# Kernel optimization log

Measured on AMD Instinct MI355X. Metric: run time of the kernel, lower is better.

The kernel has to match this reference:

```python
import jax, jax.numpy as jnp
import numpy as np

B, T, F_IN = 64, 512, 264        # batch, time, total features
NONLSTM = 8                      # trailing non-LSTM feature channels
F_LSTM = F_IN - NONLSTM          # 256 features fed to the LSTM stack
HIDDEN = [512, 512]              # stacked OptimizedLSTMCell dims
DENSE = [512, 256]
PRED, FPP = 16, 4                # predictions, features_per_prediction


def _glorot(key, shape):
    fan_in, fan_out = shape[0], shape[1]
    lim = jnp.sqrt(6.0 / (fan_in + fan_out))
    return jax.random.uniform(key, shape, jnp.float32, -lim, lim)


def setup_inputs() -> dict:
    key = jax.random.key(0)
    ks = jax.random.split(key, 16)
    inp = {"x": jax.random.normal(ks[0], (B, T, F_IN), jnp.float32)}
    # LSTM layer params: Wi [in,4H] (no bias on input proj), Wh [H,4H], b [4H]
    in_dim = F_LSTM
    for j, h in enumerate(HIDDEN):
        inp[f"Wi{j}"] = _glorot(ks[1 + 3 * j], (in_dim, 4 * h))
        inp[f"Wh{j}"] = _glorot(ks[2 + 3 * j], (h, 4 * h))
        inp[f"b{j}"] = jnp.zeros((4 * h,), jnp.float32)
        in_dim = h
    # Dense head
    d_in = HIDDEN[-1] + NONLSTM
    for i, d in enumerate(DENSE):
        inp[f"Wd{i}"] = _glorot(ks[8 + 2 * i], (d_in, d))
        inp[f"bd{i}"] = jnp.zeros((d,), jnp.float32)
        d_in = d
    inp["Wf"] = _glorot(ks[14], (d_in, PRED * FPP))
    inp["bf"] = jnp.zeros((PRED * FPP,), jnp.float32)
    return inp


def lstm_layer(x, Wi, Wh, b):
    """flax OptimizedLSTMCell scanned over time. x: [B, T, F] -> [B, T, H]."""
    Bq = x.shape[0]
    H = Wh.shape[0]
    xw = jnp.einsum('btf,fg->btg', x, Wi)  # precompute input projections

    def step(carry, z_in):
        c, h = carry
        z = z_in + h @ Wh + b
        i, f, g, o = jnp.split(z, 4, axis=-1)
        c = jax.nn.sigmoid(f) * c + jax.nn.sigmoid(i) * jnp.tanh(g)
        h = jax.nn.sigmoid(o) * jnp.tanh(c)
        return (c, h), h

    c0 = jnp.zeros((Bq, H), x.dtype)
    h0 = jnp.zeros((Bq, H), x.dtype)
    _, hs = jax.lax.scan(step, (c0, h0), jnp.swapaxes(xw, 0, 1))
    return jnp.swapaxes(hs, 0, 1)


def reference(x, Wi0, Wh0, b0, Wi1, Wh1, b1, Wd0, bd0, Wd1, bd1, Wf, bf):
    last_features = x[:, -1, -NONLSTM:]          # [B, 8]
    h = x[:, :, :-NONLSTM]                       # [B, T, 256]
    # single LSTM branch: history == T, downsample == 1
    h = lstm_layer(h, Wi0, Wh0, b0)
    h = lstm_layer(h, Wi1, Wh1, b1)
    out = h[:, -1, :]                            # [B, H]
    out = jnp.concatenate([out, last_features], axis=1)
    out = jax.nn.relu(out @ Wd0 + bd0)
    out = jax.nn.relu(out @ Wd1 + bd1)
    out = out @ Wf + bf
    out = out.reshape((-1, PRED, FPP))
    return jax.nn.sigmoid(out)
```

## Files before the change

### kernel.cpp

```cpp
#include <hip/hip_runtime.h>
#include <hip/hip_bf16.h>

typedef __hip_bfloat16 bf16;
typedef short bf16x8 __attribute__((ext_vector_type(8)));
typedef float f32x4 __attribute__((ext_vector_type(4)));
typedef unsigned long long u64;
typedef unsigned int u32;

#define MFMA16(A, B, C) __builtin_amdgcn_mfma_f32_16x16x32_bf16(A, B, C, 0, 0, 0)

__device__ __forceinline__ float sigf(float x) { return 1.f / (1.f + __expf(-x)); }
__device__ __forceinline__ float tanh_fast(float x) { return 2.f / (1.f + __expf(-2.f * x)) - 1.f; }

__device__ __forceinline__ bf16x8 ld16(const u64* p) {
  u64 lo = __hip_atomic_load(p, __ATOMIC_RELAXED, __HIP_MEMORY_SCOPE_SYSTEM);
  u64 hi = __hip_atomic_load(p + 1, __ATOMIC_RELAXED, __HIP_MEMORY_SCOPE_SYSTEM);
  union { u64 q[2]; bf16x8 v; } u;
  u.q[0] = lo; u.q[1] = hi;
  return u.v;
}

__global__ __launch_bounds__(256) void transpose_k(const float* __restrict__ W,
                                                   bf16* __restrict__ WT,
                                                   int K, int N) {
  __shared__ bf16 tile[32][33];
  const int n0 = blockIdx.x * 32, k0 = blockIdx.y * 32;
  const int c = threadIdx.x & 31, r0 = threadIdx.x >> 5;
  for (int i = 0; i < 4; ++i) {
    int r = r0 + 8 * i;
    tile[r][c] = __float2bfloat16(W[(long)(k0 + r) * N + (n0 + c)]);
  }
  __syncthreads();
  for (int i = 0; i < 4; ++i) {
    int r = r0 + 8 * i;
    WT[(long)(n0 + r) * K + (k0 + c)] = tile[c][r];
  }
}

__device__ __forceinline__ void gather16(const u64* __restrict__ mat, int m, int q,
                                         bf16x8* out) {
#pragma unroll
  for (int i = 0; i < 16; ++i) {
    const int s = i * 4 + q;
    out[i] = ld16(mat + ((long)(s << 6) + m) * 2);
  }
}

__global__ __launch_bounds__(256, 1) void lstm2_fused_k(
    const float* __restrict__ x,
    const bf16* __restrict__ WiT0, const bf16* __restrict__ WhT0,
    const float* __restrict__ bias0,
    const bf16* __restrict__ WiT1, const bf16* __restrict__ WhT1,
    const float* __restrict__ bias1,
    u64* __restrict__ h1D, u64* __restrict__ h2D,
    u32* __restrict__ sent)
{
  __shared__ short Wis[32 * 520];
  __shared__ short Whs[32 * 520];
  __shared__ float zs[32 * 66];
  __shared__ __align__(16) bf16 hstage[64 * 8];

  const int layer = blockIdx.x >> 6;
  const int w = blockIdx.x & 63;
  const int tid = threadIdx.x;
  const int lane = tid & 63;
  const int wv = tid >> 6;
  const int q = lane >> 4;
  const int r = lane & 15;

  const int K_in = layer ? 512 : 256;
  const bf16* WiT = layer ? WiT1 : WiT0;
  const bf16* WhT = layer ? WhT1 : WhT0;
  const float* bias = layer ? bias1 : bias0;
  u32* s0 = sent;
  u32* s1 = sent + 512 * 64;
  u64* hprevD = layer ? h2D : h1D;
  u64* houtD = layer ? h2D : h1D;
  u32* smy = (layer ? s1 : s0);

  for (int idx = tid; idx < 32 * 64; idx += 256) {
    const int j = idx >> 6, kc = idx & 63;
    const int zc = (j >> 3) * 512 + w * 8 + (j & 7);
    *(bf16x8*)(Whs + j * 520 + kc * 8) = *(const bf16x8*)(WhT + (long)zc * 512 + kc * 8);
  }
  const int csh = layer ? 6 : 5;
  const int cmask = (1 << csh) - 1;
  for (int idx = tid; idx < (32 << csh); idx += 256) {
    const int j = idx >> csh, kc = idx & cmask;
    const int zc = (j >> 3) * 512 + w * 8 + (j & 7);
    *(bf16x8*)(Wis + j * 520 + kc * 8) = *(const bf16x8*)(WiT + (long)zc * K_in + kc * 8);
  }

  const int m = wv * 16 + r;
  const short* wi0p = Wis + r * 520;
  const short* wi1p = Wis + (16 + r) * 520;
  const short* wh0p = Whs + r * 520;
  const short* wh1p = Whs + (16 + r) * 520;

  const int gb = tid & 63;
  const int gc0 = tid >> 6;
  float bias_r[2][4];
  for (int s = 0; s < 2; ++s)
    for (int g = 0; g < 4; ++g)
      bias_r[s][g] = bias[g * 512 + w * 8 + gc0 + 4 * s];
  float creg[2] = {0.f, 0.f};

  __syncthreads();

  for (int t = 0; t < 512; ++t) {
    f32x4 acc0 = {0.f, 0.f, 0.f, 0.f};
    f32x4 acc1 = {0.f, 0.f, 0.f, 0.f};

    if (layer == 0) {
      bf16x8 ax[8];
      const float* row = x + ((long)m * 512 + t) * 264;
#pragma unroll
      for (int i = 0; i < 8; ++i) {
        const float4 f0 = *(const float4*)(row + i * 32 + q * 8);
        const float4 f1 = *(const float4*)(row + i * 32 + q * 8 + 4);
        union { short s[8]; bf16x8 v8; } o;
        o.s[0] = __builtin_bit_cast(short, __float2bfloat16(f0.x));
        o.s[1] = __builtin_bit_cast(short, __float2bfloat16(f0.y));
        o.s[2] = __builtin_bit_cast(short, __float2bfloat16(f0.z));
        o.s[3] = __builtin_bit_cast(short, __float2bfloat16(f0.w));
        o.s[4] = __builtin_bit_cast(short, __float2bfloat16(f1.x));
        o.s[5] = __builtin_bit_cast(short, __float2bfloat16(f1.y));
        o.s[6] = __builtin_bit_cast(short, __float2bfloat16(f1.z));
        o.s[7] = __builtin_bit_cast(short, __float2bfloat16(f1.w));
        ax[i] = o.v8;
      }
#pragma unroll
      for (int i = 0; i < 8; ++i) {
        const int kk = i * 32;
        acc0 = MFMA16(ax[i], *(const bf16x8*)(wi0p + kk + q * 8), acc0);
        acc1 = MFMA16(ax[i], *(const bf16x8*)(wi1p + kk + q * 8), acc1);
      }
      if (t > 0) {
        if (tid < 64) {
          const u32* sp = s0 + (t - 1) * 64 + tid;
          while (__ballot(__hip_atomic_load(sp, __ATOMIC_RELAXED,
                                            __HIP_MEMORY_SCOPE_SYSTEM) != 0) != ~0ull)
            __builtin_amdgcn_s_sleep(2);
        }
        __syncthreads();
        bf16x8 ah[16];
        gather16(h1D + (long)(t - 1) * 8192, m, q, ah);
#pragma unroll
        for (int i = 0; i < 16; ++i) {
          const int kk = i * 32;
          acc0 = MFMA16(ah[i], *(const bf16x8*)(wh0p + kk + q * 8), acc0);
          acc1 = MFMA16(ah[i], *(const bf16x8*)(wh1p + kk + q * 8), acc1);
        }
      }
    } else {
      if (tid < 64) {
        const u32* sp = s0 + t * 64 + tid;
        while (__ballot(__hip_atomic_load(sp, __ATOMIC_RELAXED,
                                          __HIP_MEMORY_SCOPE_SYSTEM) != 0) != ~0ull)
          __builtin_amdgcn_s_sleep(2);
      }
      __syncthreads();
      bf16x8 ax[16];
      gather16(h1D + (long)t * 8192, m, q, ax);
#pragma unroll
      for (int i = 0; i < 16; ++i) {
        const int kk = i * 32;
        acc0 = MFMA16(ax[i], *(const bf16x8*)(wi0p + kk + q * 8), acc0);
        acc1 = MFMA16(ax[i], *(const bf16x8*)(wi1p + kk + q * 8), acc1);
      }
      if (t > 0) {
        if (tid < 64) {
          const u32* sp = s1 + (t - 1) * 64 + tid;
          while (__ballot(__hip_atomic_load(sp, __ATOMIC_RELAXED,
                                            __HIP_MEMORY_SCOPE_SYSTEM) != 0) != ~0ull)
            __builtin_amdgcn_s_sleep(2);
        }
        __syncthreads();
        bf16x8 ah[16];
        gather16(h2D + (long)(t - 1) * 8192, m, q, ah);
#pragma unroll
        for (int i = 0; i < 16; ++i) {
          const int kk = i * 32;
          acc0 = MFMA16(ah[i], *(const bf16x8*)(wh0p + kk + q * 8), acc0);
          acc1 = MFMA16(ah[i], *(const bf16x8*)(wh1p + kk + q * 8), acc1);
        }
      }
    }

    {
      const int brow = wv * 16 + q * 4;
      for (int i = 0; i < 4; ++i) zs[r * 66 + brow + i] = acc0[i];
      for (int i = 0; i < 4; ++i) zs[(16 + r) * 66 + brow + i] = acc1[i];
    }
    __syncthreads();

    for (int s = 0; s < 2; ++s) {
      const int c = gc0 + 4 * s;
      const float zi = zs[(c)*66 + gb] + bias_r[s][0];
      const float zf = zs[(8 + c) * 66 + gb] + bias_r[s][1];
      const float zg = zs[(16 + c) * 66 + gb] + bias_r[s][2];
      const float zo = zs[(24 + c) * 66 + gb] + bias_r[s][3];
      const float cnew = sigf(zf) * creg[s] + sigf(zi) * tanh_fast(zg);
      const float hnew = sigf(zo) * tanh_fast(cnew);
      creg[s] = cnew;
      hstage[gb * 8 + c] = __float2bfloat16(hnew);
    }
    __syncthreads();

    if (tid < 64) {
      const u64* src = (const u64*)(hstage + tid * 8);
      u64* dst = houtD + (((long)t * 64 + w) * 64 + tid) * 2;
      __hip_atomic_store(dst, src[0], __ATOMIC_RELAXED, __HIP_MEMORY_SCOPE_SYSTEM);
      __hip_atomic_store(dst + 1, src[1], __ATOMIC_RELAXED, __HIP_MEMORY_SCOPE_SYSTEM);
    }
    if (tid == 0)
      __hip_atomic_store(smy + t * 64 + w, 1u, __ATOMIC_RELEASE, __HIP_MEMORY_SCOPE_AGENT);
  }
}

__global__ __launch_bounds__(256) void head_k(
    const u64* __restrict__ h2D,
    const float* __restrict__ x,
    const float* __restrict__ Wd0, const float* __restrict__ bd0,
    const float* __restrict__ Wd1, const float* __restrict__ bd1,
    const float* __restrict__ Wf, const float* __restrict__ bfv,
    float* __restrict__ out) {
  const int b = blockIdx.x, tid = threadIdx.x;
  __shared__ float in0[520];
  __shared__ float d0s[512];
  __shared__ float d1s[256];
  if (tid < 64) {
    const int s = tid;
    bf16x8 v = ld16(h2D + (((long)511 * 64 + s) * 64 + b) * 2);
    union { bf16x8 v8; short sh[8]; } u;
    u.v8 = v;
    for (int j = 0; j < 8; ++j)
      in0[s * 8 + j] = __bfloat162float(__builtin_bit_cast(bf16, u.sh[j]));
  }
  if (tid < 8) in0[512 + tid] = x[((long)(b * 512 + 511)) * 264 + 256 + tid];
  __syncthreads();
  for (int j = tid; j < 512; j += 256) {
    float a = bd0[j];
    for (int k = 0; k < 520; ++k) a += in0[k] * Wd0[(long)k * 512 + j];
    d0s[j] = fmaxf(a, 0.f);
  }
  __syncthreads();
  if (tid < 256) {
    const int j = tid;
    float a = bd1[j];
    for (int k = 0; k < 512; ++k) a += d0s[k] * Wd1[(long)k * 256 + j];
    d1s[j] = fmaxf(a, 0.f);
  }
  __syncthreads();
  if (tid < 64) {
    const int j = tid;
    float a = bfv[j];
    for (int k = 0; k < 256; ++k) a += d1s[k] * Wf[(long)k * 64 + j];
    out[b * 64 + j] = sigf(a);
  }
}

extern "C" void kernel_launch(void* const* d_in, const int* in_sizes, int n_in,
                              void* d_out, int out_size, void* d_ws, size_t ws_size,
                              hipStream_t stream) {
  const float* x   = (const float*)d_in[0];
  const float* Wi0 = (const float*)d_in[1];
  const float* Wh0 = (const float*)d_in[2];
  const float* b0  = (const float*)d_in[3];
  const float* Wi1 = (const float*)d_in[4];
  const float* Wh1 = (const float*)d_in[5];
  const float* b1  = (const float*)d_in[6];
  const float* Wd0 = (const float*)d_in[7];
  const float* bd0 = (const float*)d_in[8];
  const float* Wd1 = (const float*)d_in[9];
  const float* bd1 = (const float*)d_in[10];
  const float* Wf  = (const float*)d_in[11];
  const float* bf_ = (const float*)d_in[12];
  float* out = (float*)d_out;

  char* ws = (char*)d_ws;
  size_t off = 0;
  auto carve = [&](size_t bytes) {
    void* p = ws + off;
    off += (bytes + 255) & ~(size_t)255;
    return p;
  };
  u32* sent = (u32*)carve((size_t)2 * 512 * 64 * 4);
  const size_t zero_bytes = off;
  bf16* WiT0 = (bf16*)carve((size_t)2048 * 256 * 2);
  bf16* WhT0 = (bf16*)carve((size_t)2048 * 512 * 2);
  bf16* WiT1 = (bf16*)carve((size_t)2048 * 512 * 2);
  bf16* WhT1 = (bf16*)carve((size_t)2048 * 512 * 2);
  u64*  h1D  = (u64*)carve((size_t)512 * 64 * 64 * 16);
  u64*  h2D  = (u64*)carve((size_t)512 * 64 * 64 * 16);

  hipMemsetAsync(sent, 0, zero_bytes, stream);

  transpose_k<<<dim3(2048 / 32, 256 / 32), 256, 0, stream>>>(Wi0, WiT0, 256, 2048);
  transpose_k<<<dim3(2048 / 32, 512 / 32), 256, 0, stream>>>(Wh0, WhT0, 512, 2048);
  transpose_k<<<dim3(2048 / 32, 512 / 32), 256, 0, stream>>>(Wi1, WiT1, 512, 2048);
  transpose_k<<<dim3(2048 / 32, 512 / 32), 256, 0, stream>>>(Wh1, WhT1, 512, 2048);

  lstm2_fused_k<<<128, 256, 0, stream>>>(x, WiT0, WhT0, b0, WiT1, WhT1, b1,
                                         h1D, h2D, sent);

  head_k<<<64, 256, 0, stream>>>(h2D, x, Wd0, bd0, Wd1, bd1, Wf, bf_, out);
}
```

Before: 2.954 ms.

## Split LSTM persistent kernel across batch groups with register-resident weights and split-K

The persistent two-layer LSTM kernel now runs 256 blocks instead of 128, partitioning work by layer, batch group (4 groups of 16) and 16-column gate slice. Each block syncs only on the 32 producer blocks of its own batch group rather than all 64. Recurrent weights, plus layer-0 input weights, are held in registers. The four waves split K and reduce partial sums through shared memory, and layer-1 input weights sit in XOR-swizzled LDS. The aim is to shorten the per-timestep critical path and cut the data gathered per step, at the cost of higher register pressure, more sentinels and a cross-wave reduction.

```diff
diff --git a/kernel.cpp b/kernel.cpp
--- a/kernel.cpp
+++ b/kernel.cpp
@@ -18,6 +18,19 @@
   union { u64 q[2]; bf16x8 v; } u;
   u.q[0] = lo; u.q[1] = hi;
   return u.v;
+}
+
+__device__ __forceinline__ bf16x8 pack8(float4 f0, float4 f1) {
+  union { short s[8]; bf16x8 v8; } o;
+  o.s[0] = __builtin_bit_cast(short, __float2bfloat16(f0.x));
+  o.s[1] = __builtin_bit_cast(short, __float2bfloat16(f0.y));
+  o.s[2] = __builtin_bit_cast(short, __float2bfloat16(f0.z));
+  o.s[3] = __builtin_bit_cast(short, __float2bfloat16(f0.w));
+  o.s[4] = __builtin_bit_cast(short, __float2bfloat16(f1.x));
+  o.s[5] = __builtin_bit_cast(short, __float2bfloat16(f1.y));
+  o.s[6] = __builtin_bit_cast(short, __float2bfloat16(f1.z));
+  o.s[7] = __builtin_bit_cast(short, __float2bfloat16(f1.w));
+  return o.v8;
 }
 
 __global__ __launch_bounds__(256) void transpose_k(const float* __restrict__ W,
@@ -37,15 +50,6 @@
   }
 }
 
-__device__ __forceinline__ void gather16(const u64* __restrict__ mat, int m, int q,
-                                         bf16x8* out) {
-#pragma unroll
-  for (int i = 0; i < 16; ++i) {
-    const int s = i * 4 + q;
-    out[i] = ld16(mat + ((long)(s << 6) + m) * 2);
-  }
-}
-
 __global__ __launch_bounds__(256, 1) void lstm2_fused_k(
     const float* __restrict__ x,
     const bf16* __restrict__ WiT0, const bf16* __restrict__ WhT0,
@@ -55,166 +59,174 @@
     u64* __restrict__ h1D, u64* __restrict__ h2D,
     u32* __restrict__ sent)
 {
-  __shared__ short Wis[32 * 520];
-  __shared__ short Whs[32 * 520];
-  __shared__ float zs[32 * 66];
-  __shared__ __align__(16) bf16 hstage[64 * 8];
-
-  const int layer = blockIdx.x >> 6;
-  const int w = blockIdx.x & 63;
+  __shared__ __align__(16) short Wi1s[64 * 512];
+  __shared__ float zs[4 * 64 * 20];
+  __shared__ __align__(16) bf16 hstage[256];
+
+  const int layer = blockIdx.x >> 7;
+  const int bg = (blockIdx.x >> 5) & 3;
+  const int cg = blockIdx.x & 31;
   const int tid = threadIdx.x;
   const int lane = tid & 63;
-  const int wv = tid >> 6;
+  const int kh = tid >> 6;
   const int q = lane >> 4;
   const int r = lane & 15;
 
-  const int K_in = layer ? 512 : 256;
-  const bf16* WiT = layer ? WiT1 : WiT0;
   const bf16* WhT = layer ? WhT1 : WhT0;
   const float* bias = layer ? bias1 : bias0;
   u32* s0 = sent;
-  u32* s1 = sent + 512 * 64;
-  u64* hprevD = layer ? h2D : h1D;
-  u64* houtD = layer ? h2D : h1D;
-  u32* smy = (layer ? s1 : s0);
-
-  for (int idx = tid; idx < 32 * 64; idx += 256) {
-    const int j = idx >> 6, kc = idx & 63;
-    const int zc = (j >> 3) * 512 + w * 8 + (j & 7);
-    *(bf16x8*)(Whs + j * 520 + kc * 8) = *(const bf16x8*)(WhT + (long)zc * 512 + kc * 8);
-  }
-  const int csh = layer ? 6 : 5;
-  const int cmask = (1 << csh) - 1;
-  for (int idx = tid; idx < (32 << csh); idx += 256) {
-    const int j = idx >> csh, kc = idx & cmask;
-    const int zc = (j >> 3) * 512 + w * 8 + (j & 7);
-    *(bf16x8*)(Wis + j * 520 + kc * 8) = *(const bf16x8*)(WiT + (long)zc * K_in + kc * 8);
-  }
-
-  const int m = wv * 16 + r;
-  const short* wi0p = Wis + r * 520;
-  const short* wi1p = Wis + (16 + r) * 520;
-  const short* wh0p = Whs + r * 520;
-  const short* wh1p = Whs + (16 + r) * 520;
-
-  const int gb = tid & 63;
-  const int gc0 = tid >> 6;
-  float bias_r[2][4];
-  for (int s = 0; s < 2; ++s)
-    for (int g = 0; g < 4; ++g)
-      bias_r[s][g] = bias[g * 512 + w * 8 + gc0 + 4 * s];
-  float creg[2] = {0.f, 0.f};
-
-  __syncthreads();
-
+  u32* s1 = sent + 512 * 128;
+  u32* smy = layer ? s1 : s0;
+  u64* hown = layer ? h2D : h1D;
+
+  bf16x8 wh[4][4];
+#pragma unroll
+  for (int nt = 0; nt < 4; ++nt)
+#pragma unroll
+    for (int kt = 0; kt < 4; ++kt)
+      wh[nt][kt] = *(const bf16x8*)(WhT + (long)(nt * 512 + cg * 16 + r) * 512 +
+                                    (kh * 4 + kt) * 32 + q * 8);
+
+  bf16x8 wi0r[4][2];
+  if (layer == 0) {
+#pragma unroll
+    for (int nt = 0; nt < 4; ++nt)
+#pragma unroll
+      for (int kt = 0; kt < 2; ++kt)
+        wi0r[nt][kt] = *(const bf16x8*)(WiT0 + (long)(nt * 512 + cg * 16 + r) * 256 +
+                                        (kh * 2 + kt) * 32 + q * 8);
+  } else {
+    char* wb = (char*)Wi1s;
+    for (int idx = tid; idx < 64 * 64; idx += 256) {
+      const int j = idx >> 6, kc = idx & 63;
+      const int col = (j >> 4) * 512 + cg * 16 + (j & 15);
+      *(bf16x8*)(wb + j * 1024 + ((kc ^ (j & 7)) * 16)) =
+          *(const bf16x8*)(WiT1 + (long)col * 512 + kc * 8);
+    }
+  }
+
+  const int erow = tid & 15, ec = tid >> 4;
+  float br[4];
+#pragma unroll
+  for (int g = 0; g < 4; ++g) br[g] = bias[g * 512 + cg * 16 + ec];
+  float creg = 0.f;
+
+  __syncthreads();
+
+#pragma unroll 1
   for (int t = 0; t < 512; ++t) {
-    f32x4 acc0 = {0.f, 0.f, 0.f, 0.f};
-    f32x4 acc1 = {0.f, 0.f, 0.f, 0.f};
+    f32x4 acc[4];
+#pragma unroll
+    for (int nt = 0; nt < 4; ++nt) { acc[nt][0] = 0.f; acc[nt][1] = 0.f; acc[nt][2] = 0.f; acc[nt][3] = 0.f; }
 
     if (layer == 0) {
-      bf16x8 ax[8];
-      const float* row = x + ((long)m * 512 + t) * 264;
-#pragma unroll
-      for (int i = 0; i < 8; ++i) {
-        const float4 f0 = *(const float4*)(row + i * 32 + q * 8);
-        const float4 f1 = *(const float4*)(row + i * 32 + q * 8 + 4);
-        union { short s[8]; bf16x8 v8; } o;
-        o.s[0] = __builtin_bit_cast(short, __float2bfloat16(f0.x));
-        o.s[1] = __builtin_bit_cast(short, __float2bfloat16(f0.y));
-        o.s[2] = __builtin_bit_cast(short, __float2bfloat16(f0.z));
-        o.s[3] = __builtin_bit_cast(short, __float2bfloat16(f0.w));
-        o.s[4] = __builtin_bit_cast(short, __float2bfloat16(f1.x));
-        o.s[5] = __builtin_bit_cast(short, __float2bfloat16(f1.y));
-        o.s[6] = __builtin_bit_cast(short, __float2bfloat16(f1.z));
-        o.s[7] = __builtin_bit_cast(short, __float2bfloat16(f1.w));
-        ax[i] = o.v8;
-      }
-#pragma unroll
-      for (int i = 0; i < 8; ++i) {
-        const int kk = i * 32;
-        acc0 = MFMA16(ax[i], *(const bf16x8*)(wi0p + kk + q * 8), acc0);
-        acc1 = MFMA16(ax[i], *(const bf16x8*)(wi1p + kk + q * 8), acc1);
-      }
+      const float* xrow = x + ((long)(16 * bg + r) * 512 + t) * 264;
+      float4 xf[2][2];
+#pragma unroll
+      for (int kt = 0; kt < 2; ++kt) {
+        const int f0 = (kh * 2 + kt) * 32 + q * 8;
+        xf[kt][0] = *(const float4*)(xrow + f0);
+        xf[kt][1] = *(const float4*)(xrow + f0 + 4);
+      }
+      if (t > 0 && lane < 8) {
+        const u32* sp = s0 + (long)(t - 1) * 128 + bg * 32 + kh * 8 + lane;
+        while ((__ballot(__hip_atomic_load(sp, __ATOMIC_RELAXED,
+                                           __HIP_MEMORY_SCOPE_SYSTEM) != 0) &
+                0xffull) != 0xffull)
+          __builtin_amdgcn_s_sleep(2);
+      }
+      bf16x8 ax[2];
+#pragma unroll
+      for (int kt = 0; kt < 2; ++kt) ax[kt] = pack8(xf[kt][0], xf[kt][1]);
+#pragma unroll
+      for (int nt = 0; nt < 4; ++nt)
+#pragma unroll
+        for (int kt = 0; kt < 2; ++kt)
+          acc[nt] = MFMA16(ax[kt], wi0r[nt][kt], acc[nt]);
       if (t > 0) {
-        if (tid < 64) {
-          const u32* sp = s0 + (t - 1) * 64 + tid;
-          while (__ballot(__hip_atomic_load(sp, __ATOMIC_RELAXED,
-                                            __HIP_MEMORY_SCOPE_SYSTEM) != 0) != ~0ull)
-            __builtin_amdgcn_s_sleep(2);
+        bf16x8 ah[4];
+#pragma unroll
+        for (int kt = 0; kt < 4; ++kt) {
+          const int s = (kh * 4 + kt) * 4 + q;
+          ah[kt] = ld16(h1D + (((long)(t - 1) * 4 + bg) * 64 + s) * 32 + r * 2);
         }
-        __syncthreads();
-        bf16x8 ah[16];
-        gather16(h1D + (long)(t - 1) * 8192, m, q, ah);
-#pragma unroll
-        for (int i = 0; i < 16; ++i) {
-          const int kk = i * 32;
-          acc0 = MFMA16(ah[i], *(const bf16x8*)(wh0p + kk + q * 8), acc0);
-          acc1 = MFMA16(ah[i], *(const bf16x8*)(wh1p + kk + q * 8), acc1);
+#pragma unroll
+        for (int nt = 0; nt < 4; ++nt)
+#pragma unroll
+          for (int kt = 0; kt < 4; ++kt)
+            acc[nt] = MFMA16(ah[kt], wh[nt][kt], acc[nt]);
+      }
+    } else {
+      const u64 need = (t > 0) ? 0xffffull : 0xffull;
+      if (lane < 16 && (t > 0 || lane < 8)) {
+        const u32* sp;
+        if (lane < 8) sp = s0 + (long)t * 128 + bg * 32 + kh * 8 + lane;
+        else          sp = s1 + (long)(t - 1) * 128 + bg * 32 + kh * 8 + (lane - 8);
+        while ((__ballot(__hip_atomic_load(sp, __ATOMIC_RELAXED,
+                                           __HIP_MEMORY_SCOPE_SYSTEM) != 0) &
+                need) != need)
+          __builtin_amdgcn_s_sleep(2);
+      }
+      bf16x8 a2[4], a1[4];
+      if (t > 0) {
+#pragma unroll
+        for (int kt = 0; kt < 4; ++kt) {
+          const int s = (kh * 4 + kt) * 4 + q;
+          a2[kt] = ld16(h2D + (((long)(t - 1) * 4 + bg) * 64 + s) * 32 + r * 2);
         }
       }
-    } else {
-      if (tid < 64) {
-        const u32* sp = s0 + t * 64 + tid;
-        while (__ballot(__hip_atomic_load(sp, __ATOMIC_RELAXED,
-                                          __HIP_MEMORY_SCOPE_SYSTEM) != 0) != ~0ull)
-          __builtin_amdgcn_s_sleep(2);
-      }
-      __syncthreads();
-      bf16x8 ax[16];
-      gather16(h1D + (long)t * 8192, m, q, ax);
-#pragma unroll
-      for (int i = 0; i < 16; ++i) {
-        const int kk = i * 32;
-        acc0 = MFMA16(ax[i], *(const bf16x8*)(wi0p + kk + q * 8), acc0);
-        acc1 = MFMA16(ax[i], *(const bf16x8*)(wi1p + kk + q * 8), acc1);
+#pragma unroll
+      for (int kt = 0; kt < 4; ++kt) {
+        const int s = (kh * 4 + kt) * 4 + q;
+        a1[kt] = ld16(h1D + (((long)t * 4 + bg) * 64 + s) * 32 + r * 2);
       }
       if (t > 0) {
-        if (tid < 64) {
-          const u32* sp = s1 + (t - 1) * 64 + tid;
-          while (__ballot(__hip_atomic_load(sp, __ATOMIC_RELAXED,
-                                            __HIP_MEMORY_SCOPE_SYSTEM) != 0) != ~0ull)
-            __builtin_amdgcn_s_sleep(2);
+#pragma unroll
+        for (int nt = 0; nt < 4; ++nt)
+#pragma unroll
+          for (int kt = 0; kt < 4; ++kt)
+            acc[nt] = MFMA16(a2[kt], wh[nt][kt], acc[nt]);
+      }
+      const char* wb = (const char*)Wi1s;
+#pragma unroll
+      for (int nt = 0; nt < 4; ++nt)
+#pragma unroll
+        for (int kt = 0; kt < 4; ++kt) {
+          const int kc = (kh * 4 + kt) * 4 + q;
+          const bf16x8 bfrag =
+              *(const bf16x8*)(wb + (nt * 16 + r) * 1024 + ((kc ^ (r & 7)) * 16));
+          acc[nt] = MFMA16(a1[kt], bfrag, acc[nt]);
         }
-        __syncthreads();
-        bf16x8 ah[16];
-        gather16(h2D + (long)(t - 1) * 8192, m, q, ah);
-#pragma unroll
-        for (int i = 0; i < 16; ++i) {
-          const int kk = i * 32;
-          acc0 = MFMA16(ah[i], *(const bf16x8*)(wh0p + kk + q * 8), acc0);
-          acc1 = MFMA16(ah[i], *(const bf16x8*)(wh1p + kk + q * 8), acc1);
-        }
-      }
     }
 
-    {
-      const int brow = wv * 16 + q * 4;
-      for (int i = 0; i < 4; ++i) zs[r * 66 + brow + i] = acc0[i];
-      for (int i = 0; i < 4; ++i) zs[(16 + r) * 66 + brow + i] = acc1[i];
+#pragma unroll
+    for (int nt = 0; nt < 4; ++nt)
+      *(f32x4*)(zs + (kh * 64 + nt * 16 + r) * 20 + q * 4) = acc[nt];
+    __syncthreads();
+
+    float z[4];
+#pragma unroll
+    for (int g = 0; g < 4; ++g) {
+      const float* zp = zs + (g * 16 + ec) * 20 + erow;
+      z[g] = ((zp[0] + zp[1280]) + (zp[2560] + zp[3840])) + br[g];
     }
+    const float cnew = sigf(z[1]) * creg + sigf(z[0]) * tanh_fast(z[2]);
+    const float hnew = sigf(z[3]) * tanh_fast(cnew);
+    creg = cnew;
+    hstage[(ec >> 3) * 128 + erow * 8 + (ec & 7)] = __float2bfloat16(hnew);
     __syncthreads();
 
-    for (int s = 0; s < 2; ++s) {
-      const int c = gc0 + 4 * s;
-      const float zi = zs[(c)*66 + gb] + bias_r[s][0];
-      const float zf = zs[(8 + c) * 66 + gb] + bias_r[s][1];
-      const float zg = zs[(16 + c) * 66 + gb] + bias_r[s][2];
-      const float zo = zs[(24 + c) * 66 + gb] + bias_r[s][3];
-      const float cnew = sigf(zf) * creg[s] + sigf(zi) * tanh_fast(zg);
-      const float hnew = sigf(zo) * tanh_fast(cnew);
-      creg[s] = cnew;
-      hstage[gb * 8 + c] = __float2bfloat16(hnew);
-    }
-    __syncthreads();
-
-    if (tid < 64) {
+    if (tid < 32) {
       const u64* src = (const u64*)(hstage + tid * 8);
-      u64* dst = houtD + (((long)t * 64 + w) * 64 + tid) * 2;
+      u64* dst = hown + (((long)t * 4 + bg) * 64 + cg * 2 + (tid >> 4)) * 32 +
+                 (tid & 15) * 2;
       __hip_atomic_store(dst, src[0], __ATOMIC_RELAXED, __HIP_MEMORY_SCOPE_SYSTEM);
       __hip_atomic_store(dst + 1, src[1], __ATOMIC_RELAXED, __HIP_MEMORY_SCOPE_SYSTEM);
     }
     if (tid == 0)
-      __hip_atomic_store(smy + t * 64 + w, 1u, __ATOMIC_RELEASE, __HIP_MEMORY_SCOPE_AGENT);
+      __hip_atomic_store(smy + (long)t * 128 + bg * 32 + cg, 1u, __ATOMIC_RELEASE,
+                         __HIP_MEMORY_SCOPE_AGENT);
+    asm volatile("" ::: "memory");
   }
 }
 
@@ -231,7 +243,7 @@
   __shared__ float d1s[256];
   if (tid < 64) {
     const int s = tid;
-    bf16x8 v = ld16(h2D + (((long)511 * 64 + s) * 64 + b) * 2);
+    bf16x8 v = ld16(h2D + (((long)511 * 4 + (b >> 4)) * 64 + s) * 32 + (b & 15) * 2);
     union { bf16x8 v8; short sh[8]; } u;
     u.v8 = v;
     for (int j = 0; j < 8; ++j)
@@ -285,7 +297,7 @@
     off += (bytes + 255) & ~(size_t)255;
     return p;
   };
-  u32* sent = (u32*)carve((size_t)2 * 512 * 64 * 4);
+  u32* sent = (u32*)carve((size_t)2 * 512 * 128 * 4);
   const size_t zero_bytes = off;
   bf16* WiT0 = (bf16*)carve((size_t)2048 * 256 * 2);
   bf16* WhT0 = (bf16*)carve((size_t)2048 * 512 * 2);
@@ -301,7 +313,7 @@
   transpose_k<<<dim3(2048 / 32, 512 / 32), 256, 0, stream>>>(Wi1, WiT1, 512, 2048);
   transpose_k<<<dim3(2048 / 32, 512 / 32), 256, 0, stream>>>(Wh1, WhT1, 512, 2048);
 
-  lstm2_fused_k<<<128, 256, 0, stream>>>(x, WiT0, WhT0, b0, WiT1, WhT1, b1,
+  lstm2_fused_k<<<256, 256, 0, stream>>>(x, WiT0, WhT0, b0, WiT1, WhT1, b1,
                                          h1D, h2D, sent);
 
   head_k<<<64, 256, 0, stream>>>(h2D, x, Wd0, bd0, Wd1, bd1, Wf, bf_, out);
```

Result: slower. 4.359 ms (+47.5%).

## Replace sentinel flags with in-band 0xFF poison values for h handoff

Applied to the files above, without the earlier changes.

Removes the per-timestep flag array and its spin-wait and syncthreads barriers. The h buffers are now pre-filled with 0xFF, and each lane polls its own loaded h values until they stop being the poison pattern, so data and readiness arrive in one load. Loads of the previous h are issued early, before the input MFMAs, to overlap their latency. The cost is a much larger memset of both h buffers (about 64MB), and correctness depends on each 8-byte word being written atomically and on no real bf16 data ever equalling all ones.

```diff
diff --git a/kernel.cpp b/kernel.cpp
--- a/kernel.cpp
+++ b/kernel.cpp
@@ -18,6 +18,19 @@
   union { u64 q[2]; bf16x8 v; } u;
   u.q[0] = lo; u.q[1] = hi;
   return u.v;
+}
+
+__device__ __forceinline__ bf16x8 pack8(float4 f0, float4 f1) {
+  union { short s[8]; bf16x8 v8; } o;
+  o.s[0] = __builtin_bit_cast(short, __float2bfloat16(f0.x));
+  o.s[1] = __builtin_bit_cast(short, __float2bfloat16(f0.y));
+  o.s[2] = __builtin_bit_cast(short, __float2bfloat16(f0.z));
+  o.s[3] = __builtin_bit_cast(short, __float2bfloat16(f0.w));
+  o.s[4] = __builtin_bit_cast(short, __float2bfloat16(f1.x));
+  o.s[5] = __builtin_bit_cast(short, __float2bfloat16(f1.y));
+  o.s[6] = __builtin_bit_cast(short, __float2bfloat16(f1.z));
+  o.s[7] = __builtin_bit_cast(short, __float2bfloat16(f1.w));
+  return o.v8;
 }
 
 __global__ __launch_bounds__(256) void transpose_k(const float* __restrict__ W,
@@ -37,12 +50,28 @@
   }
 }
 
-__device__ __forceinline__ void gather16(const u64* __restrict__ mat, int m, int q,
-                                         bf16x8* out) {
+__device__ __forceinline__ void gather16_issue(const u64* __restrict__ mat, int m,
+                                               int q, bf16x8* out) {
 #pragma unroll
   for (int i = 0; i < 16; ++i) {
     const int s = i * 4 + q;
     out[i] = ld16(mat + ((long)(s << 6) + m) * 2);
+  }
+}
+
+__device__ __forceinline__ void validate16(const u64* __restrict__ mat, int m,
+                                           int q, bf16x8* out) {
+#pragma unroll
+  for (int i = 0; i < 16; ++i) {
+    const u64* p = mat + ((long)((i * 4 + q) << 6) + m) * 2;
+    union { bf16x8 v; u64 w[2]; } u;
+    u.v = out[i];
+    while (u.w[0] == ~0ull || u.w[1] == ~0ull) {
+      __builtin_amdgcn_s_sleep(1);
+      u.w[0] = __hip_atomic_load(p, __ATOMIC_RELAXED, __HIP_MEMORY_SCOPE_SYSTEM);
+      u.w[1] = __hip_atomic_load(p + 1, __ATOMIC_RELAXED, __HIP_MEMORY_SCOPE_SYSTEM);
+    }
+    out[i] = u.v;
   }
 }
 
@@ -52,8 +81,7 @@
     const float* __restrict__ bias0,
     const bf16* __restrict__ WiT1, const bf16* __restrict__ WhT1,
     const float* __restrict__ bias1,
-    u64* __restrict__ h1D, u64* __restrict__ h2D,
-    u32* __restrict__ sent)
+    u64* __restrict__ h1D, u64* __restrict__ h2D)
 {
   __shared__ short Wis[32 * 520];
   __shared__ short Whs[32 * 520];
@@ -72,11 +100,7 @@
   const bf16* WiT = layer ? WiT1 : WiT0;
   const bf16* WhT = layer ? WhT1 : WhT0;
   const float* bias = layer ? bias1 : bias0;
-  u32* s0 = sent;
-  u32* s1 = sent + 512 * 64;
-  u64* hprevD = layer ? h2D : h1D;
   u64* houtD = layer ? h2D : h1D;
-  u32* smy = (layer ? s1 : s0);
 
   for (int idx = tid; idx < 32 * 64; idx += 256) {
     const int j = idx >> 6, kc = idx & 63;
@@ -107,44 +131,30 @@
 
   __syncthreads();
 
+#pragma unroll 1
   for (int t = 0; t < 512; ++t) {
     f32x4 acc0 = {0.f, 0.f, 0.f, 0.f};
     f32x4 acc1 = {0.f, 0.f, 0.f, 0.f};
 
     if (layer == 0) {
-      bf16x8 ax[8];
       const float* row = x + ((long)m * 512 + t) * 264;
+      float4 xf0[8], xf1[8];
 #pragma unroll
       for (int i = 0; i < 8; ++i) {
-        const float4 f0 = *(const float4*)(row + i * 32 + q * 8);
-        const float4 f1 = *(const float4*)(row + i * 32 + q * 8 + 4);
-        union { short s[8]; bf16x8 v8; } o;
-        o.s[0] = __builtin_bit_cast(short, __float2bfloat16(f0.x));
-        o.s[1] = __builtin_bit_cast(short, __float2bfloat16(f0.y));
-        o.s[2] = __builtin_bit_cast(short, __float2bfloat16(f0.z));
-        o.s[3] = __builtin_bit_cast(short, __float2bfloat16(f0.w));
-        o.s[4] = __builtin_bit_cast(short, __float2bfloat16(f1.x));
-        o.s[5] = __builtin_bit_cast(short, __float2bfloat16(f1.y));
-        o.s[6] = __builtin_bit_cast(short, __float2bfloat16(f1.z));
-        o.s[7] = __builtin_bit_cast(short, __float2bfloat16(f1.w));
-        ax[i] = o.v8;
-      }
+        xf0[i] = *(const float4*)(row + i * 32 + q * 8);
+        xf1[i] = *(const float4*)(row + i * 32 + q * 8 + 4);
+      }
+      bf16x8 ah[16];
+      if (t > 0) gather16_issue(h1D + (long)(t - 1) * 8192, m, q, ah);
 #pragma unroll
       for (int i = 0; i < 8; ++i) {
+        const bf16x8 ax = pack8(xf0[i], xf1[i]);
         const int kk = i * 32;
-        acc0 = MFMA16(ax[i], *(const bf16x8*)(wi0p + kk + q * 8), acc0);
-        acc1 = MFMA16(ax[i], *(const bf16x8*)(wi1p + kk + q * 8), acc1);
+        acc0 = MFMA16(ax, *(const bf16x8*)(wi0p + kk + q * 8), acc0);
+        acc1 = MFMA16(ax, *(const bf16x8*)(wi1p + kk + q * 8), acc1);
       }
       if (t > 0) {
-        if (tid < 64) {
-          const u32* sp = s0 + (t - 1) * 64 + tid;
-          while (__ballot(__hip_atomic_load(sp, __ATOMIC_RELAXED,
-                                            __HIP_MEMORY_SCOPE_SYSTEM) != 0) != ~0ull)
-            __builtin_amdgcn_s_sleep(2);
-        }
-        __syncthreads();
-        bf16x8 ah[16];
-        gather16(h1D + (long)(t - 1) * 8192, m, q, ah);
+        validate16(h1D + (long)(t - 1) * 8192, m, q, ah);
 #pragma unroll
         for (int i = 0; i < 16; ++i) {
           const int kk = i * 32;
@@ -153,15 +163,10 @@
         }
       }
     } else {
-      if (tid < 64) {
-        const u32* sp = s0 + t * 64 + tid;
-        while (__ballot(__hip_atomic_load(sp, __ATOMIC_RELAXED,
-                                          __HIP_MEMORY_SCOPE_SYSTEM) != 0) != ~0ull)
-          __builtin_amdgcn_s_sleep(2);
-      }
-      __syncthreads();
-      bf16x8 ax[16];
-      gather16(h1D + (long)t * 8192, m, q, ax);
+      bf16x8 ax[16], ah[16];
+      gather16_issue(h1D + (long)t * 8192, m, q, ax);
+      if (t > 0) gather16_issue(h2D + (long)(t - 1) * 8192, m, q, ah);
+      validate16(h1D + (long)t * 8192, m, q, ax);
 #pragma unroll
       for (int i = 0; i < 16; ++i) {
         const int kk = i * 32;
@@ -169,15 +174,7 @@
         acc1 = MFMA16(ax[i], *(const bf16x8*)(wi1p + kk + q * 8), acc1);
       }
       if (t > 0) {
-        if (tid < 64) {
-          const u32* sp = s1 + (t - 1) * 64 + tid;
-          while (__ballot(__hip_atomic_load(sp, __ATOMIC_RELAXED,
-                                            __HIP_MEMORY_SCOPE_SYSTEM) != 0) != ~0ull)
-            __builtin_amdgcn_s_sleep(2);
-        }
-        __syncthreads();
-        bf16x8 ah[16];
-        gather16(h2D + (long)(t - 1) * 8192, m, q, ah);
+        validate16(h2D + (long)(t - 1) * 8192, m, q, ah);
 #pragma unroll
         for (int i = 0; i < 16; ++i) {
           const int kk = i * 32;
@@ -213,8 +210,6 @@
       __hip_atomic_store(dst, src[0], __ATOMIC_RELAXED, __HIP_MEMORY_SCOPE_SYSTEM);
       __hip_atomic_store(dst + 1, src[1], __ATOMIC_RELAXED, __HIP_MEMORY_SCOPE_SYSTEM);
     }
-    if (tid == 0)
-      __hip_atomic_store(smy + t * 64 + w, 1u, __ATOMIC_RELEASE, __HIP_MEMORY_SCOPE_AGENT);
   }
 }
 
@@ -285,8 +280,6 @@
     off += (bytes + 255) & ~(size_t)255;
     return p;
   };
-  u32* sent = (u32*)carve((size_t)2 * 512 * 64 * 4);
-  const size_t zero_bytes = off;
   bf16* WiT0 = (bf16*)carve((size_t)2048 * 256 * 2);
   bf16* WhT0 = (bf16*)carve((size_t)2048 * 512 * 2);
   bf16* WiT1 = (bf16*)carve((size_t)2048 * 512 * 2);
@@ -294,7 +287,7 @@
   u64*  h1D  = (u64*)carve((size_t)512 * 64 * 64 * 16);
   u64*  h2D  = (u64*)carve((size_t)512 * 64 * 64 * 16);
 
-  hipMemsetAsync(sent, 0, zero_bytes, stream);
+  hipMemsetAsync(h1D, 0xFF, (size_t)2 * 512 * 64 * 64 * 16, stream);
 
   transpose_k<<<dim3(2048 / 32, 256 / 32), 256, 0, stream>>>(Wi0, WiT0, 256, 2048);
   transpose_k<<<dim3(2048 / 32, 512 / 32), 256, 0, stream>>>(Wh0, WhT0, 512, 2048);
@@ -302,7 +295,7 @@
   transpose_k<<<dim3(2048 / 32, 512 / 32), 256, 0, stream>>>(Wh1, WhT1, 512, 2048);
 
   lstm2_fused_k<<<128, 256, 0, stream>>>(x, WiT0, WhT0, b0, WiT1, WhT1, b1,
-                                         h1D, h2D, sent);
+                                         h1D, h2D);
 
   head_k<<<64, 256, 0, stream>>>(h2D, x, Wd0, bd0, Wd1, bd1, Wf, bf_, out);
 }
```

After: 3.237 ms. 1.1x slower.
